# Kernel tuning notes

Measured on AMD Instinct MI355X. Metric: run time of the kernel, lower is better.

Reference implementation:

```python
import jax, jax.numpy as jnp
import numpy as np

Z_DIM = 128
K = 64
RANK = 16
B = 65536


def setup_inputs() -> dict:
    key = jax.random.key(0)
    k1, k2, k3 = jax.random.split(key, 3)
    z = jax.random.normal(k1, (B, Z_DIM), dtype=jnp.float32)
    # nn.Linear(z_dim, K*rank): weight [K*rank, z_dim], bias [K*rank]
    bound = 1.0 / np.sqrt(Z_DIM)
    W = jax.random.uniform(k2, (K * RANK, Z_DIM), dtype=jnp.float32, minval=-bound, maxval=bound)
    b = jax.random.uniform(k3, (K * RANK,), dtype=jnp.float32, minval=-bound, maxval=bound)
    return {"z": z, "W": W, "b": b}


def reference(z, W, b):
    bsz = z.shape[0]
    # linear projection: [B, K*rank]
    w = z @ W.T + b
    w = w.reshape(bsz, K, RANK) + 1e-6
    # batched reduced QR on small K x rank matrices (fp32, like torch .float())
    q, _ = jnp.linalg.qr(w.astype(jnp.float32), mode="reduced")
    return q.astype(z.dtype)
```

## Files before the change

kernel.cpp:

```cpp
#include <hip/hip_runtime.h>

#define TOTAL_B 65536
#define NKR 1024
#define ZD 128

__global__ __launch_bounds__(256) void gemm_zwt(
    const float* __restrict__ z, const float* __restrict__ W,
    const float* __restrict__ bias, float* __restrict__ out)
{
    __shared__ float zs[32][132];
    __shared__ float ws[32][132];

    const int tid = threadIdx.x;
    const int tx = tid & 15;
    const int ty = tid >> 4;
    const int m0 = blockIdx.y * 128;
    const int n0 = blockIdx.x * 128;

    float acc[8][8];
    #pragma unroll
    for (int i = 0; i < 8; ++i)
        #pragma unroll
        for (int j = 0; j < 8; ++j) acc[i][j] = 0.f;

    const int kq = (tid & 7) * 4;
    const int mr = tid >> 3;

    const float* gz = z + (size_t)(m0 + mr) * ZD + kq;
    const float* gw = W + (size_t)(n0 + mr) * ZD + kq;

    float4 vz[4], vw[4];
    #pragma unroll
    for (int p = 0; p < 4; ++p) {
        vz[p] = *(const float4*)(gz + (size_t)p * 32 * ZD);
        vw[p] = *(const float4*)(gw + (size_t)p * 32 * ZD);
    }

    #pragma unroll
    for (int kc = 0; kc < ZD; kc += 32) {
        #pragma unroll
        for (int p = 0; p < 4; ++p) {
            int ml = mr + p * 32;
            zs[kq + 0][ml] = vz[p].x; zs[kq + 1][ml] = vz[p].y;
            zs[kq + 2][ml] = vz[p].z; zs[kq + 3][ml] = vz[p].w;
            ws[kq + 0][ml] = vw[p].x; ws[kq + 1][ml] = vw[p].y;
            ws[kq + 2][ml] = vw[p].z; ws[kq + 3][ml] = vw[p].w;
        }
        __syncthreads();

        if (kc + 32 < ZD) {
            #pragma unroll
            for (int p = 0; p < 4; ++p) {
                vz[p] = *(const float4*)(gz + (size_t)p * 32 * ZD + kc + 32);
                vw[p] = *(const float4*)(gw + (size_t)p * 32 * ZD + kc + 32);
            }
        }

        #pragma unroll 8
        for (int k = 0; k < 32; ++k) {
            float4 a0 = *(const float4*)&zs[k][ty * 4];
            float4 a1 = *(const float4*)&zs[k][64 + ty * 4];
            float4 c0 = *(const float4*)&ws[k][tx * 4];
            float4 c1 = *(const float4*)&ws[k][64 + tx * 4];
            float zr[8] = {a0.x, a0.y, a0.z, a0.w, a1.x, a1.y, a1.z, a1.w};
            float wr[8] = {c0.x, c0.y, c0.z, c0.w, c1.x, c1.y, c1.z, c1.w};
            #pragma unroll
            for (int i = 0; i < 8; ++i)
                #pragma unroll
                for (int j = 0; j < 8; ++j)
                    acc[i][j] = fmaf(zr[i], wr[j], acc[i][j]);
        }
        __syncthreads();
    }

    float bv0[4], bv1[4];
    #pragma unroll
    for (int j = 0; j < 4; ++j) {
        bv0[j] = bias[n0 + tx * 4 + j] + 1e-6f;
        bv1[j] = bias[n0 + 64 + tx * 4 + j] + 1e-6f;
    }

    #pragma unroll
    for (int i = 0; i < 8; ++i) {
        int row = (i < 4) ? (ty * 4 + i) : (64 + ty * 4 + i - 4);
        size_t base = (size_t)(m0 + row) * NKR + n0;
        float4 o0, o1;
        o0.x = acc[i][0] + bv0[0]; o0.y = acc[i][1] + bv0[1];
        o0.z = acc[i][2] + bv0[2]; o0.w = acc[i][3] + bv0[3];
        o1.x = acc[i][4] + bv1[0]; o1.y = acc[i][5] + bv1[1];
        o1.z = acc[i][6] + bv1[2]; o1.w = acc[i][7] + bv1[3];
        *(float4*)(out + base + tx * 4) = o0;
        *(float4*)(out + base + 64 + tx * 4) = o1;
    }
}

template <int CTRL>
__device__ __forceinline__ float dpp_add(float v) {
    int x = __builtin_amdgcn_update_dpp(0, __float_as_int(v), CTRL, 0xF, 0xF, false);
    return v + __int_as_float(x);
}

__device__ __forceinline__ float rsum16(float v) {
    v = dpp_add<0x128>(v);
    v = dpp_add<0x124>(v);
    v = dpp_add<0x122>(v);
    v = dpp_add<0x121>(v);
    return v;
}

__global__ __launch_bounds__(256) void qr_batched(float* __restrict__ buf)
{
    const int tid = threadIdx.x;
    const int lq = tid & 15;
    const int item = (blockIdx.x * 256 + tid) >> 4;

    float* p = buf + (size_t)item * NKR + lq * 16;

    float a[16][4];
    #pragma unroll
    for (int i = 0; i < 4; ++i) {
        #pragma unroll
        for (int cc = 0; cc < 16; cc += 4) {
            float4 v = *(const float4*)(p + i * 256 + cc);
            a[cc + 0][i] = v.x; a[cc + 1][i] = v.y;
            a[cc + 2][i] = v.z; a[cc + 3][i] = v.w;
        }
    }

    float tau[16];

    #pragma unroll
    for (int j = 0; j < 16; ++j) {
        float x0 = a[j][0], x1 = a[j][1], x2 = a[j][2], x3 = a[j][3];
        float x0m = (lq > j) ? x0 : 0.f;
        float pp = fmaf(x0m, x0m, fmaf(x1, x1, fmaf(x2, x2, x3 * x3)));
        float xn2   = rsum16(pp);
        float alpha = rsum16((lq == j) ? x0 : 0.f);

        float rr   = __builtin_amdgcn_sqrtf(fmaf(alpha, alpha, xn2));
        float beta = (alpha >= 0.f) ? -rr : rr;
        float dba  = beta - alpha;
        float tj   = dba * __builtin_amdgcn_rcpf(beta);
        float sc   = -__builtin_amdgcn_rcpf(dba);
        if (xn2 == 0.f) { tj = 0.f; sc = 0.f; }
        tau[j] = tj;

        float v0 = (lq == j) ? 1.f : ((lq > j) ? x0 * sc : 0.f);
        float v1 = x1 * sc, v2 = x2 * sc, v3 = x3 * sc;
        a[j][0] = v0; a[j][1] = v1; a[j][2] = v2; a[j][3] = v3;

        #pragma unroll
        for (int c = j + 1; c < 16; ++c) {
            float d = rsum16(fmaf(v0, a[c][0],
                        fmaf(v1, a[c][1],
                        fmaf(v2, a[c][2], v3 * a[c][3]))));
            float t = -tj * d;
            a[c][0] = fmaf(t, v0, a[c][0]);
            a[c][1] = fmaf(t, v1, a[c][1]);
            a[c][2] = fmaf(t, v2, a[c][2]);
            a[c][3] = fmaf(t, v3, a[c][3]);
        }
    }

    #pragma unroll
    for (int j = 15; j >= 0; --j) {
        float tj = tau[j];
        float v0 = a[j][0], v1 = a[j][1], v2 = a[j][2], v3 = a[j][3];
        #pragma unroll
        for (int c = j + 1; c < 16; ++c) {
            float d = rsum16(fmaf(v0, a[c][0],
                        fmaf(v1, a[c][1],
                        fmaf(v2, a[c][2], v3 * a[c][3]))));
            float t = -tj * d;
            a[c][0] = fmaf(t, v0, a[c][0]);
            a[c][1] = fmaf(t, v1, a[c][1]);
            a[c][2] = fmaf(t, v2, a[c][2]);
            a[c][3] = fmaf(t, v3, a[c][3]);
        }
        float nt = -tj;
        a[j][0] = fmaf(nt, v0, (lq == j) ? 1.f : 0.f);
        a[j][1] = nt * v1;
        a[j][2] = nt * v2;
        a[j][3] = nt * v3;
    }

    #pragma unroll
    for (int i = 0; i < 4; ++i) {
        #pragma unroll
        for (int cc = 0; cc < 16; cc += 4) {
            float4 vv = {a[cc + 0][i], a[cc + 1][i], a[cc + 2][i], a[cc + 3][i]};
            *(float4*)(p + i * 256 + cc) = vv;
        }
    }
}

extern "C" void kernel_launch(void* const* d_in, const int* in_sizes, int n_in,
                              void* d_out, int out_size, void* d_ws, size_t ws_size,
                              hipStream_t stream) {
    const float* z = (const float*)d_in[0];
    const float* W = (const float*)d_in[1];
    const float* b = (const float*)d_in[2];
    float* out = (float*)d_out;

    dim3 ggrid(NKR / 128, TOTAL_B / 128);
    hipLaunchKernelGGL(gemm_zwt, ggrid, dim3(256), 0, stream, z, W, b, out);
    hipLaunchKernelGGL(qr_batched, dim3(TOTAL_B / 16), dim3(256), 0, stream, out);
}
```

Baseline: 605.1 us.

## Swizzle GEMM LDS layout, remap blocks per XCD, and pack QR math as float2

The GEMM now XOR-swizzles its shared-memory tile columns, meant to reduce LDS bank conflicts on the transposed stores and float4 reads. Blocks are remapped so each XCD handles a contiguous band of 64 M-tiles across all 8 N-tiles, aiming for better L2 locality of z rows. The QR kernel stores its column data as float2 vectors and uses elementwise FMA so the compiler can emit packed FP32 instructions (v_pk_fma_f32), halving the VALU op count in the Householder updates. The swizzle index math adds a few integer ops, and the block remap assumes blockIdx.x is distributed round-robin across XCDs.

```diff
diff --git a/kernel.cpp b/kernel.cpp
--- a/kernel.cpp
+++ b/kernel.cpp
@@ -14,8 +14,11 @@
     const int tid = threadIdx.x;
     const int tx = tid & 15;
     const int ty = tid >> 4;
-    const int m0 = blockIdx.y * 128;
-    const int n0 = blockIdx.x * 128;
+
+    const int xcd = blockIdx.x;
+    const int seq = blockIdx.y;
+    const int m0 = (xcd * 64 + (seq >> 3)) * 128;
+    const int n0 = (seq & 7) * 128;
 
     float acc[8][8];
     #pragma unroll
@@ -25,6 +28,8 @@
 
     const int kq = (tid & 7) * 4;
     const int mr = tid >> 3;
+    const int xk = ((tid >> 2) & 2) << 2 | ((tid & 2) << 2);
+    const int xkw = (((kq >> 2) & 3) << 3);
 
     const float* gz = z + (size_t)(m0 + mr) * ZD + kq;
     const float* gw = W + (size_t)(n0 + mr) * ZD + kq;
@@ -40,7 +45,7 @@
     for (int kc = 0; kc < ZD; kc += 32) {
         #pragma unroll
         for (int p = 0; p < 4; ++p) {
-            int ml = mr + p * 32;
+            int ml = (mr + p * 32) ^ xkw;
             zs[kq + 0][ml] = vz[p].x; zs[kq + 1][ml] = vz[p].y;
             zs[kq + 2][ml] = vz[p].z; zs[kq + 3][ml] = vz[p].w;
             ws[kq + 0][ml] = vw[p].x; ws[kq + 1][ml] = vw[p].y;
@@ -58,10 +63,11 @@
 
         #pragma unroll 8
         for (int k = 0; k < 32; ++k) {
-            float4 a0 = *(const float4*)&zs[k][ty * 4];
-            float4 a1 = *(const float4*)&zs[k][64 + ty * 4];
-            float4 c0 = *(const float4*)&ws[k][tx * 4];
-            float4 c1 = *(const float4*)&ws[k][64 + tx * 4];
+            const int xkr = ((k >> 2) & 3) << 3;
+            float4 a0 = *(const float4*)&zs[k][(ty * 4) ^ xkr];
+            float4 a1 = *(const float4*)&zs[k][64 + ((ty * 4) ^ xkr)];
+            float4 c0 = *(const float4*)&ws[k][(tx * 4) ^ xkr];
+            float4 c1 = *(const float4*)&ws[k][64 + ((tx * 4) ^ xkr)];
             float zr[8] = {a0.x, a0.y, a0.z, a0.w, a1.x, a1.y, a1.z, a1.w};
             float wr[8] = {c0.x, c0.y, c0.z, c0.w, c1.x, c1.y, c1.z, c1.w};
             #pragma unroll
@@ -94,6 +100,8 @@
     }
 }
 
+typedef float f32x2 __attribute__((ext_vector_type(2)));
+
 template <int CTRL>
 __device__ __forceinline__ float dpp_add(float v) {
     int x = __builtin_amdgcn_update_dpp(0, __float_as_int(v), CTRL, 0xF, 0xF, false);
@@ -116,14 +124,20 @@
 
     float* p = buf + (size_t)item * NKR + lq * 16;
 
-    float a[16][4];
+    f32x2 a[16][2];
     #pragma unroll
     for (int i = 0; i < 4; ++i) {
+        const int h = i >> 1;
         #pragma unroll
         for (int cc = 0; cc < 16; cc += 4) {
             float4 v = *(const float4*)(p + i * 256 + cc);
-            a[cc + 0][i] = v.x; a[cc + 1][i] = v.y;
-            a[cc + 2][i] = v.z; a[cc + 3][i] = v.w;
+            if ((i & 1) == 0) {
+                a[cc + 0][h].x = v.x; a[cc + 1][h].x = v.y;
+                a[cc + 2][h].x = v.z; a[cc + 3][h].x = v.w;
+            } else {
+                a[cc + 0][h].y = v.x; a[cc + 1][h].y = v.y;
+                a[cc + 2][h].y = v.z; a[cc + 3][h].y = v.w;
+            }
         }
     }
 
@@ -131,10 +145,12 @@
 
     #pragma unroll
     for (int j = 0; j < 16; ++j) {
-        float x0 = a[j][0], x1 = a[j][1], x2 = a[j][2], x3 = a[j][3];
-        float x0m = (lq > j) ? x0 : 0.f;
-        float pp = fmaf(x0m, x0m, fmaf(x1, x1, fmaf(x2, x2, x3 * x3)));
-        float xn2   = rsum16(pp);
+        f32x2 xlo = a[j][0], xhi = a[j][1];
+        float x0 = xlo.x;
+        f32x2 mlo = xlo;
+        mlo.x = (lq > j) ? x0 : 0.f;
+        f32x2 pp2 = __builtin_elementwise_fma(mlo, mlo, xhi * xhi);
+        float xn2   = rsum16(pp2.x + pp2.y);
         float alpha = rsum16((lq == j) ? x0 : 0.f);
 
         float rr   = __builtin_amdgcn_sqrtf(fmaf(alpha, alpha, xn2));
@@ -145,50 +161,56 @@
         if (xn2 == 0.f) { tj = 0.f; sc = 0.f; }
         tau[j] = tj;
 
-        float v0 = (lq == j) ? 1.f : ((lq > j) ? x0 * sc : 0.f);
-        float v1 = x1 * sc, v2 = x2 * sc, v3 = x3 * sc;
-        a[j][0] = v0; a[j][1] = v1; a[j][2] = v2; a[j][3] = v3;
+        f32x2 v01, v23;
+        v01.x = (lq == j) ? 1.f : ((lq > j) ? x0 * sc : 0.f);
+        v01.y = xlo.y * sc;
+        v23 = xhi * sc;
+        a[j][0] = v01; a[j][1] = v23;
 
         #pragma unroll
         for (int c = j + 1; c < 16; ++c) {
-            float d = rsum16(fmaf(v0, a[c][0],
-                        fmaf(v1, a[c][1],
-                        fmaf(v2, a[c][2], v3 * a[c][3]))));
+            f32x2 d2 = __builtin_elementwise_fma(v01, a[c][0], v23 * a[c][1]);
+            float d = rsum16(d2.x + d2.y);
             float t = -tj * d;
-            a[c][0] = fmaf(t, v0, a[c][0]);
-            a[c][1] = fmaf(t, v1, a[c][1]);
-            a[c][2] = fmaf(t, v2, a[c][2]);
-            a[c][3] = fmaf(t, v3, a[c][3]);
+            f32x2 t2 = {t, t};
+            a[c][0] = __builtin_elementwise_fma(t2, v01, a[c][0]);
+            a[c][1] = __builtin_elementwise_fma(t2, v23, a[c][1]);
         }
     }
 
     #pragma unroll
     for (int j = 15; j >= 0; --j) {
         float tj = tau[j];
-        float v0 = a[j][0], v1 = a[j][1], v2 = a[j][2], v3 = a[j][3];
+        f32x2 v01 = a[j][0], v23 = a[j][1];
         #pragma unroll
         for (int c = j + 1; c < 16; ++c) {
-            float d = rsum16(fmaf(v0, a[c][0],
-                        fmaf(v1, a[c][1],
-                        fmaf(v2, a[c][2], v3 * a[c][3]))));
+            f32x2 d2 = __builtin_elementwise_fma(v01, a[c][0], v23 * a[c][1]);
+            float d = rsum16(d2.x + d2.y);
             float t = -tj * d;
-            a[c][0] = fmaf(t, v0, a[c][0]);
-            a[c][1] = fmaf(t, v1, a[c][1]);
-            a[c][2] = fmaf(t, v2, a[c][2]);
-            a[c][3] = fmaf(t, v3, a[c][3]);
+            f32x2 t2 = {t, t};
+            a[c][0] = __builtin_elementwise_fma(t2, v01, a[c][0]);
+            a[c][1] = __builtin_elementwise_fma(t2, v23, a[c][1]);
         }
         float nt = -tj;
-        a[j][0] = fmaf(nt, v0, (lq == j) ? 1.f : 0.f);
-        a[j][1] = nt * v1;
-        a[j][2] = nt * v2;
-        a[j][3] = nt * v3;
+        f32x2 nt2 = {nt, nt};
+        f32x2 e0 = {(lq == j) ? 1.f : 0.f, 0.f};
+        a[j][0] = __builtin_elementwise_fma(nt2, v01, e0);
+        a[j][1] = v23 * nt;
     }
 
     #pragma unroll
     for (int i = 0; i < 4; ++i) {
+        const int h = i >> 1;
         #pragma unroll
         for (int cc = 0; cc < 16; cc += 4) {
-            float4 vv = {a[cc + 0][i], a[cc + 1][i], a[cc + 2][i], a[cc + 3][i]};
+            float4 vv;
+            if ((i & 1) == 0) {
+                vv.x = a[cc + 0][h].x; vv.y = a[cc + 1][h].x;
+                vv.z = a[cc + 2][h].x; vv.w = a[cc + 3][h].x;
+            } else {
+                vv.x = a[cc + 0][h].y; vv.y = a[cc + 1][h].y;
+                vv.z = a[cc + 2][h].y; vv.w = a[cc + 3][h].y;
+            }
             *(float4*)(p + i * 256 + cc) = vv;
         }
     }
@@ -202,7 +224,7 @@
     const float* b = (const float*)d_in[2];
     float* out = (float*)d_out;
 
-    dim3 ggrid(NKR / 128, TOTAL_B / 128);
+    dim3 ggrid(8, 512);
     hipLaunchKernelGGL(gemm_zwt, ggrid, dim3(256), 0, stream, z, W, b, out);
     hipLaunchKernelGGL(qr_batched, dim3(TOTAL_B / 16), dim3(256), 0, stream, out);
 }
```

Result: faster. 567.0 us (-6.3%).
